# Kernel tuning notes

Hardware: AMD Instinct MI355X
Metric: run time of the kernel (lower is better)

Reference implementation:

```python
import jax, jax.numpy as jnp
import numpy as np
import math

B, L, DX, DH, DFF, N, M = 16, 1024, 2, 512, 2048, 3, 8
DK = DH // M  # 64
EPS = 1e-5


def batchnorm_pos(z):
    # fresh nn.BatchNorm1d(L, affine=False) in train mode on [B, L, DH]:
    # per-position (dim 1) mean/var over (batch, feature) axes, biased variance
    mu = jnp.mean(z, axis=(0, 2), keepdims=True)
    var = jnp.mean(jnp.square(z - mu), axis=(0, 2), keepdims=True)
    return (z - mu) / jnp.sqrt(var + EPS)


def setup_inputs() -> dict:
    key = jax.random.key(0)
    ks = jax.random.split(key, 13)
    s = lambda k, shape, scale: jax.random.normal(k, shape, dtype=jnp.float32) * scale
    return {
        "x": s(ks[0], (B, L, DX), 1.0),
        "Wh": s(ks[1], (DH, DX), 1.0 / math.sqrt(DX)),
        "bh": s(ks[2], (DH,), 0.02),
        "Wq": s(ks[3], (N, M, DK, DH), 1.0 / math.sqrt(DH)),
        "Wk": s(ks[4], (N, M, DK, DH), 1.0 / math.sqrt(DH)),
        "Wv": s(ks[5], (N, M, DK, DH), 1.0 / math.sqrt(DH)),
        "Wo": s(ks[6], (N, M, DH, DK), 1.0 / math.sqrt(DK)),
        "w_bn": s(ks[7], (N, DH), 1.0),
        "b_bn": s(ks[8], (N, DH), 1.0),
        "Wff0": s(ks[9], (N, DFF, DH), 1.0 / math.sqrt(DH)),
        "bff0": s(ks[10], (N, DFF), 0.02),
        "Wff1": s(ks[11], (N, DH, DFF), 1.0 / math.sqrt(DFF)),
        "bff1": s(ks[12], (N, DH), 0.02),
    }


def reference(x, Wh, bh, Wq, Wk, Wv, Wo, w_bn, b_bn, Wff0, bff0, Wff1, bff1):
    n_layers = Wq.shape[0]
    dk = Wq.shape[2]
    scale = 1.0 / math.sqrt(dk)
    h = jnp.einsum("bld,ed->ble", x, Wh) + bh  # [B, L, DH]
    for n in range(n_layers):
        # batched multi-head attention (replaces per-head python loop)
        q = jnp.einsum("bld,mkd->bmlk", h, Wq[n])  # [B, M, L, DK]
        k = jnp.einsum("bld,mkd->bmlk", h, Wk[n])
        v = jnp.einsum("bld,mvd->bmlv", h, Wv[n])
        scores = jnp.einsum("bmlk,bmjk->bmlj", q, k) * scale  # [B, M, L, L]
        attn = jax.nn.softmax(scores, axis=-1)
        t = jnp.einsum("bmlj,bmjv->bmlv", attn, v)
        h_mha = jnp.einsum("bmlv,mdv->bld", t, Wo[n])  # sum over heads
        h_bn = w_bn[n] * batchnorm_pos(h + h_mha) + b_bn[n]
        ff = jnp.einsum("blf,df->bld", jax.nn.relu(jnp.einsum("bld,fd->blf", h_bn, Wff0[n]) + bff0[n]), Wff1[n]) + bff1[n]
        h = w_bn[n] * batchnorm_pos(h_bn + ff) + b_bn[n]
    return h
```

## Files before the change

kernel.cpp:

```cpp
#include <hip/hip_runtime.h>
#include <hip/hip_bf16.h>
#include <math.h>

#define B_   16
#define L_   1024
#define BL_  16384
#define DH_  512
#define DFF_ 2048
#define NL_  3
#define M_   8
#define DK_  64

typedef __attribute__((ext_vector_type(8))) short bf16x8;
typedef __attribute__((ext_vector_type(4))) float f32x4;
typedef __attribute__((ext_vector_type(4))) unsigned short us4;
typedef __attribute__((ext_vector_type(8))) unsigned short us8;

__device__ __forceinline__ unsigned short f2b(float x) {
    __hip_bfloat16 h = __float2bfloat16(x);
    return *(unsigned short*)&h;
}
__device__ __forceinline__ float b2f(unsigned short u) {
    unsigned int v = ((unsigned int)u) << 16;
    return __builtin_bit_cast(float, v);
}

#define GLDS(g, l) __builtin_amdgcn_global_load_lds( \
        (const __attribute__((address_space(1))) unsigned int*)(const void*)(g), \
        (__attribute__((address_space(3))) unsigned int*)(void*)(l), 16, 0, 0)

#define QKV_T 2359296
#define WO_T  786432
#define FF_T  3145728
__global__ __launch_bounds__(256) void wprep_kernel(
    const float* __restrict__ Wq, const float* __restrict__ Wk,
    const float* __restrict__ Wv, const float* __restrict__ Wo,
    const float* __restrict__ Wff0, const float* __restrict__ Wff1,
    unsigned short* __restrict__ wqkvb3, unsigned short* __restrict__ wob3,
    unsigned short* __restrict__ wff0b3, unsigned short* __restrict__ wff1b3)
{
    int i4 = (blockIdx.x * 256 + threadIdx.x) * 4;
    const float* src;
    unsigned short* dst;
    if (i4 < QKV_T) {
        int n = i4 / 786432, r = i4 % 786432;
        if (r < 262144)      src = Wq + (size_t)n * 262144 + r;
        else if (r < 524288) src = Wk + (size_t)n * 262144 + r - 262144;
        else                 src = Wv + (size_t)n * 262144 + r - 524288;
        dst = wqkvb3 + i4;
    } else if (i4 < QKV_T + WO_T) {
        int i = i4 - QKV_T;
        int n = i / 262144, r = i % 262144;
        int d = r >> 9, mv = r & 511, mm = mv >> 6, vv = mv & 63;
        src = Wo + (size_t)n * 262144 + ((size_t)mm * 512 + d) * 64 + vv;
        dst = wob3 + i;
    } else if (i4 < QKV_T + WO_T + FF_T) {
        int i = i4 - QKV_T - WO_T;
        src = Wff0 + i;
        dst = wff0b3 + i;
    } else {
        int i = i4 - QKV_T - WO_T - FF_T;
        src = Wff1 + i;
        dst = wff1b3 + i;
    }
    float4 v = *(const float4*)src;
    us4 o;
    o.x = f2b(v.x); o.y = f2b(v.y); o.z = f2b(v.z); o.w = f2b(v.w);
    *(us4*)dst = o;
}

__global__ __launch_bounds__(256) void embed_kernel(
    const float* __restrict__ x, const float* __restrict__ Wh,
    const float* __restrict__ bh, unsigned short* __restrict__ hb)
{
    int idx = blockIdx.x * 256 + threadIdx.x;
    int bl = idx >> 7;
    int e0 = (idx & 127) * 4;
    float x0 = x[bl * 2], x1 = x[bl * 2 + 1];
    us4 o;
    #pragma unroll
    for (int r = 0; r < 4; ++r) {
        int e = e0 + r;
        float v = fmaf(x0, Wh[e * 2], fmaf(x1, Wh[e * 2 + 1], bh[e]));
        ((unsigned short*)&o)[r] = f2b(v);
    }
    *(us4*)&hb[(size_t)bl * DH_ + e0] = o;
}

__global__ __launch_bounds__(512, 4) void gemm2w_kernel(
    const unsigned short* __restrict__ A, const unsigned short* __restrict__ Bm,
    const float* __restrict__ bias, unsigned short* __restrict__ Cb,
    unsigned short* __restrict__ vT, int K, int cn, int flags, int gx)
{
    constexpr int SLOT = 32768;
    __shared__ unsigned char lds[2 * SLOT];

    const int tid  = threadIdx.x;
    const int lane = tid & 63, wid = tid >> 6;
    const int wr = wid >> 2, wc = wid & 3;
    const int fr = lane & 15, fq = lane >> 4;

    const int nwg = gridDim.x;
    const int cpx = nwg >> 3;
    const int wg  = blockIdx.x;
    const int swz = (wg & 7) * cpx + (wg >> 3);
    const int by  = swz / gx;
    const int bx  = swz - by * gx;
    const int bm0 = by * 128, bn0 = bx * 128;
    const int cxor = (fr & 7) << 4;

    const int srow  = tid >> 3;
    const int scole = ((tid & 7) ^ (srow & 7)) * 8;
    const unsigned short* Ag = A  + (size_t)(bm0 + srow) * K + scole;
    const unsigned short* Bg = Bm + (size_t)(bn0 + srow) * K + scole;

    f32x4 acc[4][2];
    #pragma unroll
    for (int i = 0; i < 4; ++i)
        #pragma unroll
        for (int j = 0; j < 2; ++j)
            acc[i][j] = (f32x4){0.f, 0.f, 0.f, 0.f};

    auto ldsA = [&](int slot, int sweep) -> void* {
        return (void*)(lds + slot * SLOT + sweep * 8192 + wid * 1024);
    };
    auto ldsB = [&](int slot, int sweep) -> void* {
        return (void*)(lds + slot * SLOT + 16384 + sweep * 8192 + wid * 1024);
    };
    auto srcA = [&](int kt, int sweep) {
        return Ag + (size_t)sweep * 64 * K + kt * 64;
    };
    auto srcB = [&](int kt, int sweep) {
        return Bg + (size_t)sweep * 64 * K + kt * 64;
    };

    const int nt = K >> 6;

    GLDS(srcB(0, 0), ldsB(0, 0)); GLDS(srcB(0, 1), ldsB(0, 1));
    GLDS(srcA(0, 0), ldsA(0, 0)); GLDS(srcA(0, 1), ldsA(0, 1));
    asm volatile("s_waitcnt vmcnt(0)" ::: "memory");
    __builtin_amdgcn_s_barrier();

    for (int kt = 0; kt < nt; ++kt) {
        const int slot = kt & 1;
        const unsigned char* sb = lds + slot * SLOT;
        const int ns = slot ^ 1;
        const bool stg = (kt + 1 < nt);
        const int kn = kt + 1;

        if (stg) {
            GLDS(srcB(kn, 0), ldsB(ns, 0)); GLDS(srcB(kn, 1), ldsB(ns, 1));
            GLDS(srcA(kn, 0), ldsA(ns, 0)); GLDS(srcA(kn, 1), ldsA(ns, 1));
        }
        bf16x8 bfr[2][2], af[2][2];
        #pragma unroll
        for (int ni = 0; ni < 2; ++ni)
            #pragma unroll
            for (int kk = 0; kk < 2; ++kk)
                bfr[ni][kk] = *(const bf16x8*)(sb + 16384 +
                    (wc * 32 + ni * 16 + fr) * 128 + ((kk * 64 + fq * 16) ^ cxor));
        #pragma unroll
        for (int mi = 0; mi < 2; ++mi)
            #pragma unroll
            for (int kk = 0; kk < 2; ++kk)
                af[mi][kk] = *(const bf16x8*)(sb +
                    (wr * 64 + mi * 16 + fr) * 128 + ((kk * 64 + fq * 16) ^ cxor));
        #pragma unroll
        for (int mi = 0; mi < 2; ++mi)
            #pragma unroll
            for (int ni = 0; ni < 2; ++ni) {
                f32x4 c = acc[mi][ni];
                c = __builtin_amdgcn_mfma_f32_16x16x32_bf16(af[mi][0], bfr[ni][0], c, 0, 0, 0);
                c = __builtin_amdgcn_mfma_f32_16x16x32_bf16(af[mi][1], bfr[ni][1], c, 0, 0, 0);
                acc[mi][ni] = c;
            }
        #pragma unroll
        for (int mi = 0; mi < 2; ++mi)
            #pragma unroll
            for (int kk = 0; kk < 2; ++kk)
                af[mi][kk] = *(const bf16x8*)(sb +
                    (wr * 64 + 32 + mi * 16 + fr) * 128 + ((kk * 64 + fq * 16) ^ cxor));
        #pragma unroll
        for (int mi = 0; mi < 2; ++mi)
            #pragma unroll
            for (int ni = 0; ni < 2; ++ni) {
                f32x4 c = acc[2 + mi][ni];
                c = __builtin_amdgcn_mfma_f32_16x16x32_bf16(af[mi][0], bfr[ni][0], c, 0, 0, 0);
                c = __builtin_amdgcn_mfma_f32_16x16x32_bf16(af[mi][1], bfr[ni][1], c, 0, 0, 0);
                acc[2 + mi][ni] = c;
            }
        if (stg) asm volatile("s_waitcnt vmcnt(0)" ::: "memory");
        __builtin_amdgcn_s_barrier();
    }

    float bj[2] = {0.f, 0.f};
    if (flags & 1) {
        #pragma unroll
        for (int ni = 0; ni < 2; ++ni)
            bj[ni] = bias[bn0 + wc * 32 + ni * 16 + fr];
    }
    bool relu = flags & 2;
    bool qkvm = flags & 4;
    #pragma unroll
    for (int am = 0; am < 4; ++am) {
        int row0 = bm0 + wr * 64 + (am >> 1) * 32 + (am & 1) * 16 + fq * 4;
        #pragma unroll
        for (int an = 0; an < 2; ++an) {
            int col = bn0 + wc * 32 + an * 16 + fr;
            float v[4];
            #pragma unroll
            for (int r = 0; r < 4; ++r) {
                v[r] = acc[am][an][r] + bj[an];
                if (relu) v[r] = fmaxf(v[r], 0.f);
            }
            if (qkvm) {
                if (col < 1024) {
                    float sc = (col < 512) ? 0.1803368801111244f : 1.0f;
                    #pragma unroll
                    for (int r = 0; r < 4; ++r)
                        Cb[(size_t)(row0 + r) * cn + col] = f2b(v[r] * sc);
                } else {
                    int mm = (col - 1024) >> 6, dd = (col - 1024) & 63;
                    int bb = row0 >> 10, l0 = row0 & 1023;
                    us4 p;
                    p.x = f2b(v[0]); p.y = f2b(v[1]); p.z = f2b(v[2]); p.w = f2b(v[3]);
                    *(us4*)&vT[((size_t)(bb * 8 + mm) * 64 + dd) * 1024 + l0] = p;
                }
            } else {
                #pragma unroll
                for (int r = 0; r < 4; ++r)
                    Cb[(size_t)(row0 + r) * cn + col] = f2b(v[r]);
            }
        }
    }
}

__global__ __launch_bounds__(256, 4) void attn_mfma_kernel(
    const unsigned short* __restrict__ qk, const unsigned short* __restrict__ vT,
    unsigned short* __restrict__ t)
{
    __shared__ unsigned short Ks[64 * 64];
    __shared__ unsigned short Vs[64 * 64];
    __shared__ unsigned short Pb[4][32 * 64];

    int tid = threadIdx.x;
    int lane = tid & 63, wid = tid >> 6;
    int fr = lane & 15, fq = lane >> 4;
    int j = blockIdx.x;
    int pair = (j & 7) * 16 + (j >> 6);
    int q0 = ((j >> 3) & 7) * 128;
    int b = pair >> 3, m = pair & 7;
    int bq = b * L_;

    size_t qbase = (size_t)(bq + q0 + wid * 32) * 1024 + m * 64;
    bf16x8 qa[2][2];
    #pragma unroll
    for (int qh = 0; qh < 2; ++qh) {
        qa[qh][0] = *(const bf16x8*)&qk[qbase + (size_t)(qh * 16 + fr) * 1024 + fq * 8];
        qa[qh][1] = *(const bf16x8*)&qk[qbase + (size_t)(qh * 16 + fr) * 1024 + 32 + fq * 8];
    }

    f32x4 oaccT[2][4];
    #pragma unroll
    for (int qh = 0; qh < 2; ++qh)
        #pragma unroll
        for (int i = 0; i < 4; ++i) oaccT[qh][i] = (f32x4){0.f, 0.f, 0.f, 0.f};
    float lsum[2] = {0.f, 0.f};

    int srow = tid >> 3;
    int c16  = tid & 7;
    int scole = (c16 ^ (srow & 7)) * 8;
    const unsigned short* kg = qk + (size_t)bq * 1024 + 512 + m * 64 + scole;
    const unsigned short* vg = vT + ((size_t)pair * 64) * 1024 + scole;
    unsigned short* pw = Pb[wid];
    const int u7 = fr & 7;

    uint4 k0 = *(const uint4*)&kg[(size_t)(srow) * 1024];
    uint4 k1 = *(const uint4*)&kg[(size_t)(srow + 32) * 1024];
    uint4 v0 = *(const uint4*)&vg[(size_t)(srow) * 1024];
    uint4 v1 = *(const uint4*)&vg[(size_t)(srow + 32) * 1024];

    for (int kt = 0; kt < L_ / 64; ++kt) {
        __syncthreads();
        *(uint4*)&Ks[(srow)      * 64 + c16 * 8] = k0;
        *(uint4*)&Ks[(srow + 32) * 64 + c16 * 8] = k1;
        *(uint4*)&Vs[(srow)      * 64 + c16 * 8] = v0;
        *(uint4*)&Vs[(srow + 32) * 64 + c16 * 8] = v1;
        __syncthreads();
        if (kt + 1 < L_ / 64) {
            int kb = (kt + 1) * 64;
            k0 = *(const uint4*)&kg[(size_t)(kb + srow) * 1024];
            k1 = *(const uint4*)&kg[(size_t)(kb + srow + 32) * 1024];
            v0 = *(const uint4*)&vg[(size_t)(srow) * 1024 + kb];
            v1 = *(const uint4*)&vg[(size_t)(srow + 32) * 1024 + kb];
        }

        __builtin_amdgcn_s_setprio(1);
        #pragma unroll
        for (int nk = 0; nk < 4; ++nk) {
            const unsigned short* krow = &Ks[(nk * 16 + fr) * 64];
            bf16x8 kf0 = *(const bf16x8*)&krow[((fq     ) ^ u7) * 8];
            bf16x8 kf1 = *(const bf16x8*)&krow[((4 + fq) ^ u7) * 8];
            #pragma unroll
            for (int qh = 0; qh < 2; ++qh) {
                f32x4 s = __builtin_amdgcn_mfma_f32_16x16x32_bf16(
                    kf0, qa[qh][0], (f32x4){0.f, 0.f, 0.f, 0.f}, 0, 0, 0);
                s = __builtin_amdgcn_mfma_f32_16x16x32_bf16(kf1, qa[qh][1], s, 0, 0, 0);
                us4 pk;
                #pragma unroll
                for (int r = 0; r < 4; ++r) {
                    float p = exp2f(s[r]);
                    lsum[qh] += p;
                    ((unsigned short*)&pk)[r] = f2b(p);
                }
                int prow = qh * 16 + fr;
                int pc16 = nk * 2 + (fq >> 1);
                int addr = prow * 128 + ((pc16 ^ (prow & 7)) << 4) + (fq & 1) * 8;
                *(us4*)((unsigned char*)pw + addr) = pk;
            }
        }
        bf16x8 pa[2][2];
        #pragma unroll
        for (int qh = 0; qh < 2; ++qh) {
            int prow = qh * 16 + fr;
            const unsigned char* pr = (const unsigned char*)pw + prow * 128;
            pa[qh][0] = *(const bf16x8*)(pr + (((fq    ) ^ (prow & 7)) << 4));
            pa[qh][1] = *(const bf16x8*)(pr + (((4 + fq) ^ (prow & 7)) << 4));
        }
        #pragma unroll
        for (int nt = 0; nt < 4; ++nt) {
            const unsigned short* vrow = &Vs[(nt * 16 + fr) * 64];
            bf16x8 vf0 = *(const bf16x8*)&vrow[((fq     ) ^ u7) * 8];
            bf16x8 vf1 = *(const bf16x8*)&vrow[((4 + fq) ^ u7) * 8];
            #pragma unroll
            for (int qh = 0; qh < 2; ++qh) {
                oaccT[qh][nt] = __builtin_amdgcn_mfma_f32_16x16x32_bf16(
                    vf0, pa[qh][0], oaccT[qh][nt], 0, 0, 0);
                oaccT[qh][nt] = __builtin_amdgcn_mfma_f32_16x16x32_bf16(
                    vf1, pa[qh][1], oaccT[qh][nt], 0, 0, 0);
            }
        }
        __builtin_amdgcn_s_setprio(0);
    }

    float inv[2];
    #pragma unroll
    for (int qh = 0; qh < 2; ++qh) {
        float s = lsum[qh];
        s += __shfl_xor(s, 16);
        s += __shfl_xor(s, 32);
        inv[qh] = 1.f / s;
    }
    #pragma unroll
    for (int qh = 0; qh < 2; ++qh) {
        size_t orow = (size_t)(bq + q0 + wid * 32 + qh * 16 + fr) * DH_ + m * 64;
        #pragma unroll
        for (int nt = 0; nt < 4; ++nt) {
            us4 ob;
            #pragma unroll
            for (int r = 0; r < 4; ++r)
                ((unsigned short*)&ob)[r] = f2b(oaccT[qh][nt][r] * inv[qh]);
            *(us4*)&t[orow + nt * 16 + fq * 4] = ob;
        }
    }
}

__global__ __launch_bounds__(256) void bn_fused_kernel(
    const unsigned short* __restrict__ a, const unsigned short* __restrict__ b,
    const float* __restrict__ w, const float* __restrict__ bias,
    unsigned short* __restrict__ outb, float* __restrict__ outf)
{
    int l = blockIdx.x, tid = threadIdx.x;
    us8 za[4], zb[4];
    size_t offs[4];
    float s = 0.f, s2 = 0.f;
    #pragma unroll
    for (int i = 0; i < 4; ++i) {
        int u = tid + i * 256;
        int bb = u >> 6, dg = (u & 63) * 8;
        size_t off = ((size_t)bb * L_ + l) * DH_ + dg;
        offs[i] = off;
        za[i] = *(const us8*)&a[off];
        zb[i] = *(const us8*)&b[off];
        #pragma unroll
        for (int jj = 0; jj < 8; ++jj) {
            float z = b2f(za[i][jj]) + b2f(zb[i][jj]);
            s += z;
            s2 = fmaf(z, z, s2);
        }
    }
    #pragma unroll
    for (int off = 32; off > 0; off >>= 1) {
        s  += __shfl_down(s, off);
        s2 += __shfl_down(s2, off);
    }
    __shared__ float red[8];
    __shared__ float mrs[2];
    int wv = tid >> 6;
    if ((tid & 63) == 0) { red[wv] = s; red[4 + wv] = s2; }
    __syncthreads();
    if (tid == 0) {
        float S  = red[0] + red[1] + red[2] + red[3];
        float S2 = red[4] + red[5] + red[6] + red[7];
        float mu  = S * (1.f / 8192.f);
        float var = S2 * (1.f / 8192.f) - mu * mu;
        mrs[0] = mu;
        mrs[1] = rsqrtf(var + 1e-5f);
    }
    __syncthreads();
    float mu = mrs[0], rs = mrs[1];
    #pragma unroll
    for (int i = 0; i < 4; ++i) {
        int u = tid + i * 256;
        int dg = (u & 63) * 8;
        float o[8];
        #pragma unroll
        for (int jj = 0; jj < 8; ++jj) {
            float z = b2f(za[i][jj]) + b2f(zb[i][jj]);
            o[jj] = fmaf(w[dg + jj], (z - mu) * rs, bias[dg + jj]);
        }
        if (outb) {
            us8 ob;
            #pragma unroll
            for (int jj = 0; jj < 8; ++jj) ob[jj] = f2b(o[jj]);
            *(us8*)&outb[offs[i]] = ob;
        }
        if (outf) {
            float4 o0 = {o[0], o[1], o[2], o[3]};
            float4 o1 = {o[4], o[5], o[6], o[7]};
            *(float4*)&outf[offs[i]]     = o0;
            *(float4*)&outf[offs[i] + 4] = o1;
        }
    }
}

extern "C" void kernel_launch(void* const* d_in, const int* in_sizes, int n_in,
                              void* d_out, int out_size, void* d_ws, size_t ws_size,
                              hipStream_t stream)
{
    const float* x    = (const float*)d_in[0];
    const float* Wh   = (const float*)d_in[1];
    const float* bh   = (const float*)d_in[2];
    const float* Wq   = (const float*)d_in[3];
    const float* Wk   = (const float*)d_in[4];
    const float* Wv   = (const float*)d_in[5];
    const float* Wo   = (const float*)d_in[6];
    const float* wbn  = (const float*)d_in[7];
    const float* bbn  = (const float*)d_in[8];
    const float* Wff0 = (const float*)d_in[9];
    const float* bff0 = (const float*)d_in[10];
    const float* Wff1 = (const float*)d_in[11];
    const float* bff1 = (const float*)d_in[12];
    float* out = (float*)d_out;

    float* st = (float*)d_ws;
    unsigned short* hb    = (unsigned short*)(st + 2048);
    unsigned short* qkkb  = hb + (size_t)BL_ * DH_;
    unsigned short* vTb   = qkkb + (size_t)BL_ * 1024;
    unsigned short* tb    = vTb + (size_t)BL_ * DH_;
    unsigned short* mhab  = tb + (size_t)BL_ * DH_;
    unsigned short* hbnb  = mhab + (size_t)BL_ * DH_;
    unsigned short* ffob  = hbnb + (size_t)BL_ * DH_;
    unsigned short* wqkvb3 = ffob + (size_t)BL_ * DH_;
    unsigned short* wob3   = wqkvb3 + QKV_T;
    unsigned short* wff0b3 = wob3 + WO_T;
    unsigned short* wff1b3 = wff0b3 + FF_T;
    unsigned short* ffmb  = qkkb;

    wprep_kernel<<<(QKV_T + WO_T + 2 * FF_T) / 1024, 256, 0, stream>>>(
        Wq, Wk, Wv, Wo, Wff0, Wff1, wqkvb3, wob3, wff0b3, wff1b3);
    embed_kernel<<<BL_ * DH_ / 4 / 256, 256, 0, stream>>>(x, Wh, bh, hb);

    const int GQKV = 12 * 128;
    const int GWO  = 4 * 128;
    const int GFF0 = 16 * 128;
    const int GFF1 = 4 * 128;

    for (int n = 0; n < NL_; ++n) {
        const unsigned short* wqkvb = wqkvb3 + (size_t)n * 786432;
        const unsigned short* wob   = wob3   + (size_t)n * 262144;
        const unsigned short* wff0b = wff0b3 + (size_t)n * 1048576;
        const unsigned short* wff1b = wff1b3 + (size_t)n * 1048576;
        const float* wbn_n  = wbn  + (size_t)n * DH_;
        const float* bbn_n  = bbn  + (size_t)n * DH_;
        const float* bff0_n = bff0 + (size_t)n * DFF_;
        const float* bff1_n = bff1 + (size_t)n * DH_;
        bool last = (n == NL_ - 1);

        gemm2w_kernel<<<GQKV, 512, 0, stream>>>(hb, wqkvb, nullptr,
            qkkb, vTb, DH_, 1024, 4, 12);
        attn_mfma_kernel<<<1024, 256, 0, stream>>>(qkkb, vTb, tb);
        gemm2w_kernel<<<GWO, 512, 0, stream>>>(tb, wob, nullptr,
            mhab, nullptr, DH_, DH_, 0, 4);
        bn_fused_kernel<<<L_, 256, 0, stream>>>(hb, mhab, wbn_n, bbn_n,
            hbnb, nullptr);
        gemm2w_kernel<<<GFF0, 512, 0, stream>>>(hbnb, wff0b, bff0_n,
            ffmb, nullptr, DH_, DFF_, 1 | 2, 16);
        gemm2w_kernel<<<GFF1, 512, 0, stream>>>(ffmb, wff1b, bff1_n,
            ffob, nullptr, DFF_, DH_, 1, 4);
        bn_fused_kernel<<<L_, 256, 0, stream>>>(hbnb, ffob, wbn_n, bbn_n,
            last ? nullptr : hb, last ? out : nullptr);
    }
}
```

Baseline: 625.9 us.

## Load V fragments directly from global in attention; hoist all A fragment loads in GEMM

In the attention kernel, V^T fragments are now read straight from global memory into registers each tile, which removes the Vs shared-memory buffer and its store/load round trip. In the GEMM main loop, all four A-fragment groups are loaded from LDS up front instead of in two halves, so the MFMA sequence can run without an intermediate LDS wait. The V change drops LDS traffic and shared-memory footprint, but each wave now fetches its own V data from global/L2 with no prefetch ahead of use, so load latency may be exposed. Every wave also duplicates the V reads. Holding more A fragments raises register pressure.

```diff
diff --git a/kernel.cpp b/kernel.cpp
--- a/kernel.cpp
+++ b/kernel.cpp
@@ -152,7 +152,7 @@
             GLDS(srcB(kn, 0), ldsB(ns, 0)); GLDS(srcB(kn, 1), ldsB(ns, 1));
             GLDS(srcA(kn, 0), ldsA(ns, 0)); GLDS(srcA(kn, 1), ldsA(ns, 1));
         }
-        bf16x8 bfr[2][2], af[2][2];
+        bf16x8 bfr[2][2], af[4][2];
         #pragma unroll
         for (int ni = 0; ni < 2; ++ni)
             #pragma unroll
@@ -160,34 +160,20 @@
                 bfr[ni][kk] = *(const bf16x8*)(sb + 16384 +
                     (wc * 32 + ni * 16 + fr) * 128 + ((kk * 64 + fq * 16) ^ cxor));
         #pragma unroll
-        for (int mi = 0; mi < 2; ++mi)
+        for (int mi = 0; mi < 4; ++mi)
             #pragma unroll
             for (int kk = 0; kk < 2; ++kk)
                 af[mi][kk] = *(const bf16x8*)(sb +
-                    (wr * 64 + mi * 16 + fr) * 128 + ((kk * 64 + fq * 16) ^ cxor));
-        #pragma unroll
-        for (int mi = 0; mi < 2; ++mi)
+                    (wr * 64 + ((mi >> 1) * 32 + (mi & 1) * 16) + fr) * 128 +
+                    ((kk * 64 + fq * 16) ^ cxor));
+        #pragma unroll
+        for (int mi = 0; mi < 4; ++mi)
             #pragma unroll
             for (int ni = 0; ni < 2; ++ni) {
                 f32x4 c = acc[mi][ni];
                 c = __builtin_amdgcn_mfma_f32_16x16x32_bf16(af[mi][0], bfr[ni][0], c, 0, 0, 0);
                 c = __builtin_amdgcn_mfma_f32_16x16x32_bf16(af[mi][1], bfr[ni][1], c, 0, 0, 0);
                 acc[mi][ni] = c;
-            }
-        #pragma unroll
-        for (int mi = 0; mi < 2; ++mi)
-            #pragma unroll
-            for (int kk = 0; kk < 2; ++kk)
-                af[mi][kk] = *(const bf16x8*)(sb +
-                    (wr * 64 + 32 + mi * 16 + fr) * 128 + ((kk * 64 + fq * 16) ^ cxor));
-        #pragma unroll
-        for (int mi = 0; mi < 2; ++mi)
-            #pragma unroll
-            for (int ni = 0; ni < 2; ++ni) {
-                f32x4 c = acc[2 + mi][ni];
-                c = __builtin_amdgcn_mfma_f32_16x16x32_bf16(af[mi][0], bfr[ni][0], c, 0, 0, 0);
-                c = __builtin_amdgcn_mfma_f32_16x16x32_bf16(af[mi][1], bfr[ni][1], c, 0, 0, 0);
-                acc[2 + mi][ni] = c;
             }
         if (stg) asm volatile("s_waitcnt vmcnt(0)" ::: "memory");
         __builtin_amdgcn_s_barrier();
@@ -240,7 +226,6 @@
     unsigned short* __restrict__ t)
 {
     __shared__ unsigned short Ks[64 * 64];
-    __shared__ unsigned short Vs[64 * 64];
     __shared__ unsigned short Pb[4][32 * 64];
 
     int tid = threadIdx.x;
@@ -271,28 +256,30 @@
     int c16  = tid & 7;
     int scole = (c16 ^ (srow & 7)) * 8;
     const unsigned short* kg = qk + (size_t)bq * 1024 + 512 + m * 64 + scole;
-    const unsigned short* vg = vT + ((size_t)pair * 64) * 1024 + scole;
+    const unsigned short* vrow0 = vT + ((size_t)pair * 64 + fr) * 1024;
     unsigned short* pw = Pb[wid];
     const int u7 = fr & 7;
 
     uint4 k0 = *(const uint4*)&kg[(size_t)(srow) * 1024];
     uint4 k1 = *(const uint4*)&kg[(size_t)(srow + 32) * 1024];
-    uint4 v0 = *(const uint4*)&vg[(size_t)(srow) * 1024];
-    uint4 v1 = *(const uint4*)&vg[(size_t)(srow + 32) * 1024];
 
     for (int kt = 0; kt < L_ / 64; ++kt) {
+        int kb = kt * 64;
         __syncthreads();
         *(uint4*)&Ks[(srow)      * 64 + c16 * 8] = k0;
         *(uint4*)&Ks[(srow + 32) * 64 + c16 * 8] = k1;
-        *(uint4*)&Vs[(srow)      * 64 + c16 * 8] = v0;
-        *(uint4*)&Vs[(srow + 32) * 64 + c16 * 8] = v1;
         __syncthreads();
+        bf16x8 vfr[4][2];
+        #pragma unroll
+        for (int nt = 0; nt < 4; ++nt) {
+            const unsigned short* vr = vrow0 + (size_t)(nt * 16) * 1024 + kb;
+            vfr[nt][0] = *(const bf16x8*)&vr[fq * 8];
+            vfr[nt][1] = *(const bf16x8*)&vr[32 + fq * 8];
+        }
         if (kt + 1 < L_ / 64) {
-            int kb = (kt + 1) * 64;
-            k0 = *(const uint4*)&kg[(size_t)(kb + srow) * 1024];
-            k1 = *(const uint4*)&kg[(size_t)(kb + srow + 32) * 1024];
-            v0 = *(const uint4*)&vg[(size_t)(srow) * 1024 + kb];
-            v1 = *(const uint4*)&vg[(size_t)(srow + 32) * 1024 + kb];
+            int kn = (kt + 1) * 64;
+            k0 = *(const uint4*)&kg[(size_t)(kn + srow) * 1024];
+            k1 = *(const uint4*)&kg[(size_t)(kn + srow + 32) * 1024];
         }
 
         __builtin_amdgcn_s_setprio(1);
@@ -329,15 +316,12 @@
         }
         #pragma unroll
         for (int nt = 0; nt < 4; ++nt) {
-            const unsigned short* vrow = &Vs[(nt * 16 + fr) * 64];
-            bf16x8 vf0 = *(const bf16x8*)&vrow[((fq     ) ^ u7) * 8];
-            bf16x8 vf1 = *(const bf16x8*)&vrow[((4 + fq) ^ u7) * 8];
             #pragma unroll
             for (int qh = 0; qh < 2; ++qh) {
                 oaccT[qh][nt] = __builtin_amdgcn_mfma_f32_16x16x32_bf16(
-                    vf0, pa[qh][0], oaccT[qh][nt], 0, 0, 0);
+                    vfr[nt][0], pa[qh][0], oaccT[qh][nt], 0, 0, 0);
                 oaccT[qh][nt] = __builtin_amdgcn_mfma_f32_16x16x32_bf16(
-                    vf1, pa[qh][1], oaccT[qh][nt], 0, 0, 0);
+                    vfr[nt][1], pa[qh][1], oaccT[qh][nt], 0, 0, 0);
             }
         }
         __builtin_amdgcn_s_setprio(0);
```

Result: slower. 796.7 us (+27.3%).
